# Optimization experiments

Measured on AMD Instinct MI355X. Metric: run time of the kernel, lower is better.

Reference implementation:

```python
import jax, jax.numpy as jnp
import numpy as np

DEPTH = 4  # init kwarg 'depth'
H = 256   # init kwarg 'hidden_size'
ATOM_FDIM, BOND_FDIM = 35, 5


def _build_graph(rng, N, E):
    src = rng.integers(0, N, E).astype(np.int32)
    dst = rng.integers(0, N, E).astype(np.int32)
    # line graph (backtracking=False): lg edge e1 -> e2 iff dst[e1]==src[e2] and src[e1]!=dst[e2]
    indeg = np.bincount(dst, minlength=N)
    idx_sorted = np.argsort(dst, kind='stable')          # edge ids grouped by dst node
    ptr = np.concatenate([[0], np.cumsum(indeg)]).astype(np.int64)
    counts = indeg[src]                                   # in-edges of src[e] feed edge e
    total = int(counts.sum())
    lg_dst = np.repeat(np.arange(E, dtype=np.int64), counts)
    cum = np.cumsum(counts) - counts
    within = np.arange(total) - np.repeat(cum, counts)
    lg_src = idx_sorted[np.repeat(ptr[src], counts) + within]
    keep = src[lg_src] != dst[lg_dst]                     # drop backtracking pairs
    return src, dst, lg_src[keep].astype(np.int32), lg_dst[keep].astype(np.int32)


def setup_inputs() -> dict:
    rng = np.random.default_rng(0)
    N, E, Et, K, G = 50000, 200000, 100000, 50000, 2000
    src, dst, lg_src, lg_dst = _build_graph(rng, N, E)
    graph_ids = ((np.arange(N, dtype=np.int64) * G) // N).astype(np.int32)
    f32 = lambda *s: rng.standard_normal(s).astype(np.float32)
    return {
        'x_nodes': jnp.asarray(f32(N, ATOM_FDIM)),
        'x_edges': jnp.asarray(rng.random((E, BOND_FDIM)).astype(np.float32)),
        'tree_m': jnp.asarray(f32(Et, H) * 0.1),
        'W_i': jnp.asarray(f32(ATOM_FDIM + BOND_FDIM, H) * 0.05),
        'W_h': jnp.asarray(f32(H, H) * 0.05),
        'W_o': jnp.asarray(f32(ATOM_FDIM + H, H) * 0.05),
        'b_o': jnp.asarray(f32(H) * 0.05),
        'edge_src': jnp.asarray(src),
        'edge_dst': jnp.asarray(dst),
        'lg_src': jnp.asarray(lg_src),
        'lg_dst': jnp.asarray(lg_dst),
        'tgt_nodes': jnp.asarray(rng.integers(0, N, K).astype(np.int32)),
        'tree_eid': jnp.asarray(rng.integers(0, Et, K).astype(np.int32)),
        'graph_ids': jnp.asarray(graph_ids),
        'n_graphs': G,
    }


def reference(x_nodes, x_edges, tree_m, W_i, W_h, W_o, b_o,
              edge_src, edge_dst, lg_src, lg_dst, tgt_nodes, tree_eid,
              graph_ids, n_graphs):
    N = x_nodes.shape[0]
    E = x_edges.shape[0]
    # edge input features: [src atom feats | bond feats] @ W_i (no bias)
    msg_input = jnp.concatenate([x_nodes[edge_src], x_edges], axis=1) @ W_i  # [E,H]
    msg = jax.nn.relu(msg_input)
    # tree message alignment: scatter-add tree edge messages onto cand nodes
    node_alpha = jnp.zeros((N, msg.shape[1]), msg.dtype).at[tgt_nodes].add(tree_m[tree_eid])
    edge_alpha = node_alpha[edge_src]  # apply_edges: alpha = src alpha
    # loopy BP over the line graph
    for _ in range(DEPTH - 1):
        accum = jax.ops.segment_sum(msg[lg_src], lg_dst, num_segments=E)  # [E,H]
        msg = jax.nn.relu(msg_input + (accum + edge_alpha) @ W_h)
    # gather: m = sum of incoming edge messages per node
    m = jax.ops.segment_sum(msg, edge_dst, num_segments=N)  # [N,H]
    h = jax.nn.relu(jnp.concatenate([x_nodes, m + node_alpha], axis=1) @ W_o + b_o)
    # mean_nodes per candidate graph
    sums = jax.ops.segment_sum(h, graph_ids, num_segments=n_graphs)
    cnt = jax.ops.segment_sum(jnp.ones((N, 1), h.dtype), graph_ids, num_segments=n_graphs)
    return sums / jnp.maximum(cnt, 1.0)
```

## Files before the change

### kernel.cpp

```cpp
#include <hip/hip_runtime.h>
#include <stdint.h>

typedef unsigned short u16;
typedef __attribute__((ext_vector_type(8))) short bf16x8;
typedef __attribute__((ext_vector_type(4))) float f32x4;

#define HD 256
#define AST 328
#define CORR_CAP 8192

static __device__ __forceinline__ float b2f(u16 x){
  union{float f; unsigned u;} v; v.u = ((unsigned)x)<<16; return v.f;
}
static __device__ __forceinline__ u16 f2b(float f){
  union{float f; unsigned u;} v; v.f = f;
  unsigned r = v.u + 0x7fffu + ((v.u>>16)&1u);
  return (u16)(r>>16);
}
static __device__ __forceinline__ void acc4(float* a, uint2 v){
  a[0] += b2f((u16)v.x); a[1] += b2f((u16)(v.x>>16));
  a[2] += b2f((u16)v.y); a[3] += b2f((u16)(v.y>>16));
}

__global__ void k_zero_int(int* __restrict__ p, int n){
  int i = blockIdx.x*256 + threadIdx.x;
  if (i < n) p[i] = 0;
}

__global__ void k_hist(const int* __restrict__ key, int* __restrict__ deg, int n){
  int i = blockIdx.x*256 + threadIdx.x;
  if (i < n) atomicAdd(&deg[key[i]], 1);
}

__global__ void k_scan_p1(const int* __restrict__ deg, int n, int* __restrict__ bsum){
  int i = blockIdx.x*256 + threadIdx.x;
  int v = (i < n) ? deg[i] : 0;
  #pragma unroll
  for (int o=32; o>0; o>>=1) v += __shfl_down(v, o);
  __shared__ int w[4];
  if ((threadIdx.x&63)==0) w[threadIdx.x>>6] = v;
  __syncthreads();
  if (threadIdx.x==0) bsum[blockIdx.x] = w[0]+w[1]+w[2]+w[3];
}
__global__ __launch_bounds__(1024) void k_scan_p2(int* __restrict__ bsum, int nb,
                                                  int* __restrict__ total_dst){
  __shared__ int sm[1024];
  int t = threadIdx.x;
  int v = (t < nb) ? bsum[t] : 0;
  sm[t] = v; __syncthreads();
  for (int o=1; o<1024; o<<=1){
    int u = (t>=o) ? sm[t-o] : 0;
    __syncthreads();
    sm[t] += u;
    __syncthreads();
  }
  if (t < nb) bsum[t] = sm[t] - v;
  if (t == 1023 && total_dst) *total_dst = sm[1023];
}
__global__ void k_scan_p3(const int* __restrict__ deg, const int* __restrict__ bsum, int n,
                          int* __restrict__ start, int* __restrict__ cursor){
  int t = threadIdx.x;
  int i = blockIdx.x*256 + t;
  int v = (i < n) ? deg[i] : 0;
  __shared__ int sm[256];
  sm[t] = v; __syncthreads();
  for (int o=1; o<256; o<<=1){
    int u = (t>=o) ? sm[t-o] : 0;
    __syncthreads();
    sm[t] += u;
    __syncthreads();
  }
  int ex = sm[t] - v + bsum[blockIdx.x];
  if (i < n){ start[i] = ex; cursor[i] = ex; }
}

__global__ void k_fill(const int* __restrict__ key, const int* __restrict__ val,
                       int* __restrict__ cursor, int* __restrict__ bucket, int n){
  int i = blockIdx.x*256 + threadIdx.x;
  if (i >= n) return;
  int pos = atomicAdd(&cursor[key[i]], 1);
  bucket[pos] = val ? val[i] : i;
}

__global__ void k_permarr(const int* __restrict__ perm, const int* __restrict__ esrc,
                          const int* __restrict__ edst, int* __restrict__ esrc_p,
                          int* __restrict__ edst_p, int E){
  int e = blockIdx.x*256 + threadIdx.x;
  if (e >= E) return;
  int o = perm[e];
  esrc_p[e] = esrc[o];
  edst_p[e] = edst[o];
}

__global__ void k_feat_e(const float* __restrict__ xn, const float* __restrict__ xe,
                         const int* __restrict__ perm, const int* __restrict__ esrc_p,
                         u16* __restrict__ feat, int E){
  int g = blockIdx.x*256 + threadIdx.x;
  int e = g >> 6, c = g & 63;
  if (e >= E) return;
  float v = 0.f;
  if (c < 35) v = xn[(size_t)esrc_p[e]*35 + c];
  else if (c < 40) v = xe[(size_t)perm[e]*5 + (c-35)];
  feat[g] = f2b(v);
}
__global__ void k_xnf(const float* __restrict__ xn, u16* __restrict__ xnf, int N){
  int g = blockIdx.x*256 + threadIdx.x;
  int v2 = g >> 6, c = g & 63;
  if (v2 >= N) return;
  float v = (c < 35) ? xn[(size_t)v2*35 + c] : 0.f;
  xnf[g] = f2b(v);
}

__global__ void k_alpha_gather(const float* __restrict__ tree_m, const int* __restrict__ start,
                               const int* __restrict__ bucket, u16* __restrict__ alpha16, int N){
  int v = (int)(((long long)blockIdx.x*blockDim.x + threadIdx.x)>>6);
  int l = threadIdx.x & 63;
  if (v >= N) return;
  int s = start[v], e2 = start[v+1];
  float a0=0.f,a1=0.f,a2=0.f,a3=0.f;
  for (int j=s;j<e2;j++){
    float4 tv = *(const float4*)(tree_m + (size_t)bucket[j]*HD + l*4);
    a0 += tv.x; a1 += tv.y; a2 += tv.z; a3 += tv.w;
  }
  ushort4 o; o.x=f2b(a0); o.y=f2b(a1); o.z=f2b(a2); o.w=f2b(a3);
  *(ushort4*)(alpha16 + (size_t)v*HD + l*4) = o;
}

__global__ void k_nodesum(const u16* __restrict__ msg, const u16* __restrict__ alpha16,
                          const int* __restrict__ start_d, u16* __restrict__ nodeacc, int N){
  int v = (int)(((long long)blockIdx.x*blockDim.x + threadIdx.x)>>6);
  int l = threadIdx.x & 63;
  if (v >= N) return;
  int s = start_d[v], e2 = start_d[v+1];
  float a[4];
  { uint2 av = *(const uint2*)(alpha16 + (size_t)v*HD + l*4);
    a[0]=b2f((u16)av.x); a[1]=b2f((u16)(av.x>>16));
    a[2]=b2f((u16)av.y); a[3]=b2f((u16)(av.y>>16)); }
  const u16* ml = msg + (size_t)s*HD + l*4;
  int cnt = e2 - s;
  int j = 0;
  for (; j+2 <= cnt; j+=2){
    uint2 v0 = *(const uint2*)(ml);
    uint2 v1 = *(const uint2*)(ml + HD);
    ml += 2*HD;
    acc4(a, v0); acc4(a, v1);
  }
  for (; j < cnt; j++){
    uint2 v0 = *(const uint2*)(ml); ml += HD;
    acc4(a, v0);
  }
  ushort4 o; o.x=f2b(a[0]); o.y=f2b(a[1]); o.z=f2b(a[2]); o.w=f2b(a[3]);
  *(ushort4*)(nodeacc + (size_t)v*HD + l*4) = o;
}

__global__ void k_pairs(const int* __restrict__ esrc_p, const int* __restrict__ edst_p,
                        const int* __restrict__ start_d,
                        int* __restrict__ npairs, int2* __restrict__ pairs, int E){
  int e = blockIdx.x*256 + threadIdx.x;
  if (e >= E) return;
  int u = esrc_p[e], v = edst_p[e];
  int s = start_d[u], t = start_d[u+1];
  for (int ep=s; ep<t; ep++){
    if (esrc_p[ep] == v){
      int pos = atomicAdd(npairs, 1);
      if (pos < CORR_CAP) pairs[pos] = (int2){e, ep};
    }
  }
}

__global__ void k_snapshot(const u16* __restrict__ msg, const int2* __restrict__ pairs,
                           const int* __restrict__ npairs_p, u16* __restrict__ corrbuf){
  int np = *npairs_p; if (np > CORR_CAP) np = CORR_CAP;
  int wid = (blockIdx.x*256 + threadIdx.x) >> 6;
  int l = threadIdx.x & 63;
  int nw = gridDim.x * 4;
  for (int p = wid; p < np; p += nw){
    int ep = pairs[p].y;
    *(uint2*)(corrbuf + (size_t)p*HD + l*4) =
        *(const uint2*)(msg + (size_t)ep*HD + l*4);
  }
}

__global__ __launch_bounds__(256) void k_fixup(
    const float* __restrict__ xn, const float* __restrict__ xe,
    const int* __restrict__ perm, const int* __restrict__ esrc_p,
    const u16* __restrict__ nacc, const u16* __restrict__ corrbuf,
    const int2* __restrict__ pairs, const int* __restrict__ npairs_p,
    const float* __restrict__ Wi, const float* __restrict__ Wh, u16* __restrict__ msg){
  int np = *npairs_p; if (np > CORR_CAP) np = CORR_CAP;
  int t = threadIdx.x;
  __shared__ float cs[256];
  for (int p = blockIdx.x; p < np; p += gridDim.x){
    int e = pairs[p].x;
    bool first = true;
    for (int q=0;q<p;q++) if (pairs[q].x == e){ first = false; break; }
    if (!first) continue;
    int u = esrc_p[e];
    float c = 0.f;
    for (int q=p;q<np;q++) if (pairs[q].x == e) c += b2f(corrbuf[(size_t)q*HD + t]);
    cs[t] = c; __syncthreads();
    float acc = 0.f;
    for (int k=0;k<35;k++) acc += xn[(size_t)u*35 + k] * Wi[k*HD + t];
    int oe = perm[e];
    for (int k=0;k<5;k++)  acc += xe[(size_t)oe*5 + k] * Wi[(35+k)*HD + t];
    for (int k=0;k<HD;k++) acc += (b2f(nacc[(size_t)u*HD + k]) - cs[k]) * Wh[k*HD + t];
    msg[(size_t)e*HD + t] = f2b(acc > 0.f ? acc : 0.f);
    __syncthreads();
  }
}

__global__ void k_prep_B(const float* __restrict__ Wi, const float* __restrict__ Wh,
                         const float* __restrict__ Wo,
                         u16* __restrict__ BTf_bp, u16* __restrict__ BTf_fo){
  int g = blockIdx.x*256 + threadIdx.x;
  if (g >= 81920) return;
  int i = g & 7;
  int l = (g>>3) & 63;
  int t = g >> 9;
  int nj = t & 15, ks = t >> 4;
  int n = nj*16 + (l & 15);
  int k = ks*32 + (l>>4)*8 + i;
  float bp = 0.f, fo = 0.f;
  if (k < 40) bp = Wi[k*HD + n];
  else if (k >= 64) bp = Wh[(k-64)*HD + n];
  if (k < 35) fo = Wo[k*HD + n];
  else if (k >= 64) fo = Wo[(k-29)*HD + n];
  BTf_bp[g] = f2b(bp);
  BTf_fo[g] = f2b(fo);
}

__global__ __launch_bounds__(512, 4) void k_mpnn(
    const u16* __restrict__ featA, const u16* __restrict__ nacc,
    const int* __restrict__ esrc,
    const u16* __restrict__ BTf, const float* __restrict__ bias,
    u16* __restrict__ out16, float* __restrict__ out32, int M, int mode)
{
  __shared__ u16 A_lds[16][AST];
  const int tid = threadIdx.x;
  const int w = tid>>6, l = tid&63;
  const int lr = l&15, lq = l>>4;
  const int nks = (mode==0) ? 2 : 10;
  const int nrb = (M+15)>>4;
  const int gstep = gridDim.x;

  bf16x8 Breg0[10], Breg1[10];
  #pragma unroll
  for (int ks=0; ks<10; ks++){
    if (ks < nks){
      Breg0[ks] = *(const bf16x8*)(BTf + (size_t)((ks*16 + w*2    )*512) + l*8);
      Breg1[ks] = *(const bf16x8*)(BTf + (size_t)((ks*16 + w*2 + 1)*512) + l*8);
    }
  }

  const int c0 = (w*2)*16 + lr, c1 = (w*2+1)*16 + lr;
  float b0 = 0.f, b1 = 0.f;
  if (mode == 2){ b0 = bias[c0]; b1 = bias[c1]; }

  uint2 fA={0,0}, fB={0,0}, nA={0,0}, nB={0,0};
  int rb = blockIdx.x;

  if (rb < nrb){
    int rr0 = rb*16 + w*2;
    int r0 = min(rr0, M-1), r1 = min(rr0+1, M-1);
    if (l < 16){
      fA = *(const uint2*)(featA + (size_t)r0*64 + l*4);
      fB = *(const uint2*)(featA + (size_t)r1*64 + l*4);
    }
    if (mode != 0){
      int s0 = esrc ? esrc[r0] : r0;
      int s1 = esrc ? esrc[r1] : r1;
      nA = *(const uint2*)(nacc + (size_t)s0*HD + l*4);
      nB = *(const uint2*)(nacc + (size_t)s1*HD + l*4);
    }
    if (l < 16){
      *(uint2*)&A_lds[w*2  ][l*4] = fA;
      *(uint2*)&A_lds[w*2+1][l*4] = fB;
    }
    if (mode != 0){
      *(uint2*)&A_lds[w*2  ][64 + l*4] = nA;
      *(uint2*)&A_lds[w*2+1][64 + l*4] = nB;
    }
  }
  __syncthreads();

  for (; rb < nrb; rb += gstep){
    int rbn = rb + gstep;
    if (rbn < nrb){
      int rr0 = rbn*16 + w*2;
      int r0 = min(rr0, M-1), r1 = min(rr0+1, M-1);
      if (l < 16){
        fA = *(const uint2*)(featA + (size_t)r0*64 + l*4);
        fB = *(const uint2*)(featA + (size_t)r1*64 + l*4);
      }
      if (mode != 0){
        int s0 = esrc ? esrc[r0] : r0;
        int s1 = esrc ? esrc[r1] : r1;
        nA = *(const uint2*)(nacc + (size_t)s0*HD + l*4);
        nB = *(const uint2*)(nacc + (size_t)s1*HD + l*4);
      }
    }

    f32x4 acc0 = (f32x4){0.f,0.f,0.f,0.f};
    f32x4 acc1 = (f32x4){0.f,0.f,0.f,0.f};
    const u16* Ar = &A_lds[lr][0];
    #pragma unroll
    for (int ks=0; ks<10; ks++){
      if (ks < nks){
        bf16x8 a = *(const bf16x8*)(Ar + ks*32 + lq*8);
        acc0 = __builtin_amdgcn_mfma_f32_16x16x32_bf16(a, Breg0[ks], acc0, 0,0,0);
        acc1 = __builtin_amdgcn_mfma_f32_16x16x32_bf16(a, Breg1[ks], acc1, 0,0,0);
      }
    }

    int m0 = rb*16;
    if (mode == 2){
      #pragma unroll
      for (int reg=0; reg<4; reg++){
        int gm = m0 + lq*4 + reg;
        if (gm < M){
          float v0 = acc0[reg] + b0, v1 = acc1[reg] + b1;
          out32[(size_t)gm*HD + c0] = v0 > 0.f ? v0 : 0.f;
          out32[(size_t)gm*HD + c1] = v1 > 0.f ? v1 : 0.f;
        }
      }
    } else {
      #pragma unroll
      for (int reg=0; reg<4; reg++){
        int gm = m0 + lq*4 + reg;
        if (gm < M){
          float v0 = acc0[reg], v1 = acc1[reg];
          out16[(size_t)gm*HD + c0] = f2b(v0 > 0.f ? v0 : 0.f);
          out16[(size_t)gm*HD + c1] = f2b(v1 > 0.f ? v1 : 0.f);
        }
      }
    }

    __syncthreads();
    if (rbn < nrb){
      if (l < 16){
        *(uint2*)&A_lds[w*2  ][l*4] = fA;
        *(uint2*)&A_lds[w*2+1][l*4] = fB;
      }
      if (mode != 0){
        *(uint2*)&A_lds[w*2  ][64 + l*4] = nA;
        *(uint2*)&A_lds[w*2+1][64 + l*4] = nB;
      }
    }
    __syncthreads();
  }
}

__global__ void k_graph_mean(const float* __restrict__ h, const int* __restrict__ gid,
                             int N, int G, float* __restrict__ out){
  int g = (int)(((long long)blockIdx.x*blockDim.x + threadIdx.x)>>6);
  int l = threadIdx.x & 63;
  if (g >= G) return;
  int lo=0, hi=N;
  while (lo<hi){ int mid=(lo+hi)>>1; if (gid[mid] < g) lo=mid+1; else hi=mid; }
  int b = lo;
  hi = N;
  while (lo<hi){ int mid=(lo+hi)>>1; if (gid[mid] < g+1) lo=mid+1; else hi=mid; }
  int e2 = lo;
  float a0=0.f,a1=0.f,a2=0.f,a3=0.f;
  for (int v=b; v<e2; v++){
    float4 hv = *(const float4*)(h + (size_t)v*HD + l*4);
    a0 += hv.x; a1 += hv.y; a2 += hv.z; a3 += hv.w;
  }
  int cnt = e2 - b; if (cnt < 1) cnt = 1;
  float inv = 1.0f/(float)cnt;
  float4 o; o.x=a0*inv; o.y=a1*inv; o.z=a2*inv; o.w=a3*inv;
  *(float4*)(out + (size_t)g*HD + l*4) = o;
}

extern "C" void kernel_launch(void* const* d_in, const int* in_sizes, int n_in,
                              void* d_out, int out_size, void* d_ws, size_t ws_size,
                              hipStream_t stream){
  const float* x_nodes = (const float*)d_in[0];
  const float* x_edges = (const float*)d_in[1];
  const float* tree_m  = (const float*)d_in[2];
  const float* W_i     = (const float*)d_in[3];
  const float* W_h     = (const float*)d_in[4];
  const float* W_o     = (const float*)d_in[5];
  const float* b_o     = (const float*)d_in[6];
  const int* edge_src = (const int*)d_in[7];
  const int* edge_dst = (const int*)d_in[8];
  const int* tgt      = (const int*)d_in[11];
  const int* teid     = (const int*)d_in[12];
  const int* gid      = (const int*)d_in[13];

  const int N = in_sizes[0]/35;
  const int E = in_sizes[1]/5;
  const int K = in_sizes[11];
  const int G = out_size/HD;

  char* wsb = (char*)d_ws;
  auto align256 = [](size_t x){ return (x + 255) & ~(size_t)255; };
  size_t oMsg    = 0;
  size_t oAlpha  = oMsg    + align256((size_t)E*HD*2);
  size_t oNacc   = oAlpha  + align256((size_t)N*HD*2);
  size_t oFeatE  = oNacc   + align256((size_t)N*HD*2);
  size_t oXnf    = oFeatE  + align256((size_t)E*64*2);
  size_t oBTbp   = oXnf    + align256((size_t)N*64*2);
  size_t oBTfo   = oBTbp   + align256((size_t)81920*2);
  size_t oDegD   = oBTfo   + align256((size_t)81920*2);
  size_t oStartD = oDegD   + align256((size_t)(N+1)*4);
  size_t oCurD   = oStartD + align256((size_t)(N+1)*4);
  size_t oPerm   = oCurD   + align256((size_t)N*4);
  size_t oEsrcP  = oPerm   + align256((size_t)E*4);
  size_t oEdstP  = oEsrcP  + align256((size_t)E*4);
  size_t oDegT   = oEdstP  + align256((size_t)E*4);
  size_t oStartT = oDegT   + align256((size_t)N*4);
  size_t oCurT   = oStartT + align256((size_t)(N+1)*4);
  size_t oBukT   = oCurT   + align256((size_t)N*4);
  size_t oBsum   = oBukT   + align256((size_t)K*4);
  size_t oPairs  = oBsum   + align256((size_t)1024*4);
  size_t oCorrB  = oPairs  + align256((size_t)CORR_CAP*8);

  u16*   msg     = (u16*)(wsb + oMsg);
  u16*   alpha16 = (u16*)(wsb + oAlpha);
  u16*   nacc    = (u16*)(wsb + oNacc);
  u16*   feat_e  = (u16*)(wsb + oFeatE);
  u16*   xnf     = (u16*)(wsb + oXnf);
  u16*   BTf_bp  = (u16*)(wsb + oBTbp);
  u16*   BTf_fo  = (u16*)(wsb + oBTfo);
  int*   deg_d   = (int*)(wsb + oDegD);
  int*   npairs  = deg_d + N;
  int*   start_d = (int*)(wsb + oStartD);
  int*   cur_d   = (int*)(wsb + oCurD);
  int*   perm    = (int*)(wsb + oPerm);
  int*   esrc_p  = (int*)(wsb + oEsrcP);
  int*   edst_p  = (int*)(wsb + oEdstP);
  int*   deg_t   = (int*)(wsb + oDegT);
  int*   start_t = (int*)(wsb + oStartT);
  int*   cur_t   = (int*)(wsb + oCurT);
  int*   buk_t   = (int*)(wsb + oBukT);
  int*   bsum    = (int*)(wsb + oBsum);
  int2*  pairs   = (int2*)(wsb + oPairs);
  u16*   corrbuf = (u16*)(wsb + oCorrB);
  float* hbuf    = (float*)(wsb + oMsg);

  const int egrid256 = (E+255)/256;
  const int kgrid256 = (K+255)/256;
  const int ngrid256 = (N+255)/256;
  const int nbN      = (N+255)/256;

  k_prep_B<<<320, 256, 0, stream>>>(W_i, W_h, W_o, BTf_bp, BTf_fo);

  k_zero_int<<<(N+1+255)/256, 256, 0, stream>>>(deg_d, N+1);
  k_hist<<<egrid256, 256, 0, stream>>>(edge_dst, deg_d, E);
  k_scan_p1<<<nbN, 256, 0, stream>>>(deg_d, N, bsum);
  k_scan_p2<<<1, 1024, 0, stream>>>(bsum, nbN, start_d + N);
  k_scan_p3<<<nbN, 256, 0, stream>>>(deg_d, bsum, N, start_d, cur_d);
  k_fill<<<egrid256, 256, 0, stream>>>(edge_dst, (const int*)0, cur_d, perm, E);
  k_permarr<<<egrid256, 256, 0, stream>>>(perm, edge_src, edge_dst, esrc_p, edst_p, E);
  k_feat_e<<<((size_t)E*64+255)/256, 256, 0, stream>>>(x_nodes, x_edges, perm, esrc_p, feat_e, E);
  k_xnf<<<((size_t)N*64+255)/256, 256, 0, stream>>>(x_nodes, xnf, N);

  k_zero_int<<<ngrid256, 256, 0, stream>>>(deg_t, N);
  k_hist<<<kgrid256, 256, 0, stream>>>(tgt, deg_t, K);
  k_scan_p1<<<nbN, 256, 0, stream>>>(deg_t, N, bsum);
  k_scan_p2<<<1, 1024, 0, stream>>>(bsum, nbN, start_t + N);
  k_scan_p3<<<nbN, 256, 0, stream>>>(deg_t, bsum, N, start_t, cur_t);
  k_fill<<<kgrid256, 256, 0, stream>>>(tgt, teid, cur_t, buk_t, K);
  k_alpha_gather<<<(N+3)/4, 256, 0, stream>>>(tree_m, start_t, buk_t, alpha16, N);

  k_pairs<<<egrid256, 256, 0, stream>>>(esrc_p, edst_p, start_d, npairs, pairs, E);

  k_mpnn<<<512, 512, 0, stream>>>(feat_e, (const u16*)0, (const int*)0,
                                  BTf_bp, (const float*)0, msg, (float*)0, E, 0);
  for (int it=0; it<3; ++it){
    k_nodesum<<<(N+3)/4, 256, 0, stream>>>(msg, alpha16, start_d, nacc, N);
    k_snapshot<<<32, 256, 0, stream>>>(msg, pairs, npairs, corrbuf);
    k_mpnn<<<512, 512, 0, stream>>>(feat_e, nacc, esrc_p,
                                    BTf_bp, (const float*)0, msg, (float*)0, E, 1);
    k_fixup<<<64, 256, 0, stream>>>(x_nodes, x_edges, perm, esrc_p, nacc, corrbuf,
                                    pairs, npairs, W_i, W_h, msg);
  }
  k_nodesum<<<(N+3)/4, 256, 0, stream>>>(msg, alpha16, start_d, nacc, N);
  k_mpnn<<<512, 512, 0, stream>>>(xnf, nacc, (const int*)0,
                                  BTf_fo, b_o, (u16*)0, hbuf, N, 2);
  k_graph_mean<<<(G+3)/4, 256, 0, stream>>>(hbuf, gid, N, G, (float*)d_out);
}
```

Baseline: 655.6 us.

## Hoist per-node GEMMs out of edge loop via linearity, fuse nodesum with GEMM

The W_h and W_i products depend only on the source node, apart from the bond features and a sparse backtracking correction. The change computes them once per node (N rows) instead of once per edge (E rows). A fused node kernel sums incoming messages into LDS and runs the MFMA GEMM against W_h, adding a precomputed x_nodes@W_i term. A light elementwise edge kernel then gathers U[src], adds the 5-wide bond term and applies relu. The risks are that the correction pair capacity drops to 2048, which could truncate fixups, and that rounding changes because the intermediate U is stored as bf16.

```diff
diff --git a/kernel.cpp b/kernel.cpp
--- a/kernel.cpp
+++ b/kernel.cpp
@@ -6,8 +6,8 @@
 typedef __attribute__((ext_vector_type(4))) float f32x4;
 
 #define HD 256
-#define AST 328
-#define CORR_CAP 8192
+#define AST 264
+#define CORR_CAP 2048
 
 static __device__ __forceinline__ float b2f(u16 x){
   union{float f; unsigned u;} v; v.u = ((unsigned)x)<<16; return v.f;
@@ -92,17 +92,15 @@
   edst_p[e] = edst[o];
 }
 
-__global__ void k_feat_e(const float* __restrict__ xn, const float* __restrict__ xe,
-                         const int* __restrict__ perm, const int* __restrict__ esrc_p,
-                         u16* __restrict__ feat, int E){
-  int g = blockIdx.x*256 + threadIdx.x;
-  int e = g >> 6, c = g & 63;
+__global__ void k_xep(const float* __restrict__ xe, const int* __restrict__ perm,
+                      float* __restrict__ xep, int E){
+  int e = blockIdx.x*256 + threadIdx.x;
   if (e >= E) return;
-  float v = 0.f;
-  if (c < 35) v = xn[(size_t)esrc_p[e]*35 + c];
-  else if (c < 40) v = xe[(size_t)perm[e]*5 + (c-35)];
-  feat[g] = f2b(v);
-}
+  int o = perm[e];
+  #pragma unroll
+  for (int k=0;k<5;k++) xep[(size_t)e*5+k] = xe[(size_t)o*5+k];
+}
+
 __global__ void k_xnf(const float* __restrict__ xn, u16* __restrict__ xnf, int N){
   int g = blockIdx.x*256 + threadIdx.x;
   int v2 = g >> 6, c = g & 63;
@@ -126,31 +124,164 @@
   *(ushort4*)(alpha16 + (size_t)v*HD + l*4) = o;
 }
 
-__global__ void k_nodesum(const u16* __restrict__ msg, const u16* __restrict__ alpha16,
-                          const int* __restrict__ start_d, u16* __restrict__ nodeacc, int N){
-  int v = (int)(((long long)blockIdx.x*blockDim.x + threadIdx.x)>>6);
-  int l = threadIdx.x & 63;
-  if (v >= N) return;
-  int s = start_d[v], e2 = start_d[v+1];
-  float a[4];
-  { uint2 av = *(const uint2*)(alpha16 + (size_t)v*HD + l*4);
-    a[0]=b2f((u16)av.x); a[1]=b2f((u16)(av.x>>16));
-    a[2]=b2f((u16)av.y); a[3]=b2f((u16)(av.y>>16)); }
-  const u16* ml = msg + (size_t)s*HD + l*4;
-  int cnt = e2 - s;
-  int j = 0;
-  for (; j+2 <= cnt; j+=2){
-    uint2 v0 = *(const uint2*)(ml);
-    uint2 v1 = *(const uint2*)(ml + HD);
-    ml += 2*HD;
-    acc4(a, v0); acc4(a, v1);
-  }
-  for (; j < cnt; j++){
-    uint2 v0 = *(const uint2*)(ml); ml += HD;
-    acc4(a, v0);
-  }
-  ushort4 o; o.x=f2b(a[0]); o.y=f2b(a[1]); o.z=f2b(a[2]); o.w=f2b(a[3]);
-  *(ushort4*)(nodeacc + (size_t)v*HD + l*4) = o;
+__global__ void k_prep_frag(const float* __restrict__ W, int k0, int kmax, int nks,
+                            u16* __restrict__ out){
+  int g = blockIdx.x*256 + threadIdx.x;
+  if (g >= nks*16*512) return;
+  int i = g & 7, l = (g>>3)&63, t = g>>9;
+  int nj = t & 15, ks = t >> 4;
+  int n = nj*16 + (l&15);
+  int k = ks*32 + (l>>4)*8 + i;
+  float v = (k < kmax) ? W[(size_t)(k0+k)*HD + n] : 0.f;
+  out[g] = f2b(v);
+}
+
+__global__ __launch_bounds__(512, 4) void k_pr_gemm(
+    const u16* __restrict__ featA, const u16* __restrict__ BTf,
+    u16* __restrict__ out16, int M)
+{
+  const int tid = threadIdx.x;
+  const int w = tid>>6, l = tid&63;
+  const int lr = l&15, lq = l>>4;
+  const int nrb = (M+15)>>4;
+  bf16x8 B0[2], B1[2];
+  #pragma unroll
+  for (int ks=0; ks<2; ks++){
+    B0[ks] = *(const bf16x8*)(BTf + (size_t)((ks*16 + w*2  )*512) + l*8);
+    B1[ks] = *(const bf16x8*)(BTf + (size_t)((ks*16 + w*2+1)*512) + l*8);
+  }
+  const int c0 = w*32 + lr, c1 = w*32 + 16 + lr;
+  for (int rb = blockIdx.x; rb < nrb; rb += gridDim.x){
+    int r = rb*16 + lr; int rc = min(r, M-1);
+    const u16* fr = featA + (size_t)rc*64 + lq*8;
+    bf16x8 a0 = *(const bf16x8*)(fr);
+    bf16x8 a1 = *(const bf16x8*)(fr + 32);
+    f32x4 acc0 = (f32x4){0.f,0.f,0.f,0.f};
+    f32x4 acc1 = (f32x4){0.f,0.f,0.f,0.f};
+    acc0 = __builtin_amdgcn_mfma_f32_16x16x32_bf16(a0, B0[0], acc0, 0,0,0);
+    acc0 = __builtin_amdgcn_mfma_f32_16x16x32_bf16(a1, B0[1], acc0, 0,0,0);
+    acc1 = __builtin_amdgcn_mfma_f32_16x16x32_bf16(a0, B1[0], acc1, 0,0,0);
+    acc1 = __builtin_amdgcn_mfma_f32_16x16x32_bf16(a1, B1[1], acc1, 0,0,0);
+    #pragma unroll
+    for (int reg=0; reg<4; reg++){
+      int gm = rb*16 + lq*4 + reg;
+      if (gm < M){
+        out16[(size_t)gm*HD + c0] = f2b(acc0[reg]);
+        out16[(size_t)gm*HD + c1] = f2b(acc1[reg]);
+      }
+    }
+  }
+}
+
+__global__ __launch_bounds__(512, 4) void k_nodeU(
+    const u16* __restrict__ msg, const u16* __restrict__ alpha16,
+    const int* __restrict__ start_d, const u16* __restrict__ BTf,
+    const u16* __restrict__ Padd, const float* __restrict__ bias,
+    u16* __restrict__ out16, float* __restrict__ out32, int N, int mode)
+{
+  __shared__ u16 A_lds[16][AST];
+  const int tid = threadIdx.x;
+  const int w = tid>>6, l = tid&63;
+  const int lr = l&15, lq = l>>4;
+  const int ngrp = (N+15)>>4;
+
+  bf16x8 B0[8], B1[8];
+  #pragma unroll
+  for (int ks=0; ks<8; ks++){
+    B0[ks] = *(const bf16x8*)(BTf + (size_t)((ks*16 + w*2  )*512) + l*8);
+    B1[ks] = *(const bf16x8*)(BTf + (size_t)((ks*16 + w*2+1)*512) + l*8);
+  }
+  const int c0 = w*32 + lr, c1 = w*32 + 16 + lr;
+  float b0 = 0.f, b1 = 0.f;
+  if (mode == 1){ b0 = bias[c0]; b1 = bias[c1]; }
+
+  for (int grp = blockIdx.x; grp < ngrp; grp += gridDim.x){
+    const int vb = grp*16;
+    #pragma unroll
+    for (int h=0; h<2; h++){
+      int v = vb + w*2 + h;
+      float a[4] = {0.f,0.f,0.f,0.f};
+      if (v < N){
+        uint2 av = *(const uint2*)(alpha16 + (size_t)v*HD + l*4);
+        a[0]=b2f((u16)av.x); a[1]=b2f((u16)(av.x>>16));
+        a[2]=b2f((u16)av.y); a[3]=b2f((u16)(av.y>>16));
+        int s = start_d[v], e2 = start_d[v+1];
+        const u16* ml = msg + (size_t)s*HD + l*4;
+        int cnt = e2 - s, j = 0;
+        for (; j+2 <= cnt; j+=2){
+          uint2 v0 = *(const uint2*)(ml);
+          uint2 v1 = *(const uint2*)(ml + HD);
+          ml += 2*HD;
+          acc4(a, v0); acc4(a, v1);
+        }
+        for (; j < cnt; j++){
+          uint2 v0 = *(const uint2*)(ml); ml += HD;
+          acc4(a, v0);
+        }
+      }
+      ushort4 o; o.x=f2b(a[0]); o.y=f2b(a[1]); o.z=f2b(a[2]); o.w=f2b(a[3]);
+      *(ushort4*)&A_lds[w*2+h][l*4] = o;
+    }
+    __syncthreads();
+    f32x4 acc0 = (f32x4){0.f,0.f,0.f,0.f};
+    f32x4 acc1 = (f32x4){0.f,0.f,0.f,0.f};
+    const u16* Ar = &A_lds[lr][0];
+    #pragma unroll
+    for (int ks=0; ks<8; ks++){
+      bf16x8 af = *(const bf16x8*)(Ar + ks*32 + lq*8);
+      acc0 = __builtin_amdgcn_mfma_f32_16x16x32_bf16(af, B0[ks], acc0, 0,0,0);
+      acc1 = __builtin_amdgcn_mfma_f32_16x16x32_bf16(af, B1[ks], acc1, 0,0,0);
+    }
+    #pragma unroll
+    for (int reg=0; reg<4; reg++){
+      int gm = vb + lq*4 + reg;
+      if (gm < N){
+        float v0 = acc0[reg] + b2f(Padd[(size_t)gm*HD + c0]);
+        float v1 = acc1[reg] + b2f(Padd[(size_t)gm*HD + c1]);
+        if (mode == 1){
+          v0 += b0; v1 += b1;
+          out32[(size_t)gm*HD + c0] = v0 > 0.f ? v0 : 0.f;
+          out32[(size_t)gm*HD + c1] = v1 > 0.f ? v1 : 0.f;
+        } else {
+          out16[(size_t)gm*HD + c0] = f2b(v0);
+          out16[(size_t)gm*HD + c1] = f2b(v1);
+        }
+      }
+    }
+    __syncthreads();
+  }
+}
+
+__global__ __launch_bounds__(256, 8) void k_edge_update(
+    const u16* __restrict__ U, const float* __restrict__ xep,
+    const int* __restrict__ esrc_p, const float* __restrict__ Wi,
+    u16* __restrict__ msg, int E)
+{
+  const int l = threadIdx.x & 63;
+  const int wid = (blockIdx.x*256 + threadIdx.x) >> 6;
+  const int nw = gridDim.x*4;
+  float wq[5][4];
+  #pragma unroll
+  for (int k=0;k<5;k++){
+    float4 t = *(const float4*)(Wi + (size_t)(35+k)*HD + l*4);
+    wq[k][0]=t.x; wq[k][1]=t.y; wq[k][2]=t.z; wq[k][3]=t.w;
+  }
+  for (int e = wid; e < E; e += nw){
+    int s = esrc_p[e];
+    const float* xp = xep + (size_t)e*5;
+    float x0=xp[0], x1=xp[1], x2=xp[2], x3=xp[3], x4=xp[4];
+    uint2 uv = *(const uint2*)(U + (size_t)s*HD + l*4);
+    float v[4] = { b2f((u16)uv.x), b2f((u16)(uv.x>>16)),
+                   b2f((u16)uv.y), b2f((u16)(uv.y>>16)) };
+    #pragma unroll
+    for (int j=0;j<4;j++){
+      float q = x0*wq[0][j] + x1*wq[1][j] + x2*wq[2][j] + x3*wq[3][j] + x4*wq[4][j];
+      float r = v[j] + q;
+      v[j] = r > 0.f ? r : 0.f;
+    }
+    ushort4 o; o.x=f2b(v[0]); o.y=f2b(v[1]); o.z=f2b(v[2]); o.w=f2b(v[3]);
+    *(ushort4*)(msg + (size_t)e*HD + l*4) = o;
+  }
 }
 
 __global__ void k_pairs(const int* __restrict__ esrc_p, const int* __restrict__ edst_p,
@@ -182,11 +313,11 @@
 }
 
 __global__ __launch_bounds__(256) void k_fixup(
-    const float* __restrict__ xn, const float* __restrict__ xe,
-    const int* __restrict__ perm, const int* __restrict__ esrc_p,
-    const u16* __restrict__ nacc, const u16* __restrict__ corrbuf,
-    const int2* __restrict__ pairs, const int* __restrict__ npairs_p,
-    const float* __restrict__ Wi, const float* __restrict__ Wh, u16* __restrict__ msg){
+    const u16* __restrict__ U, const float* __restrict__ xep,
+    const int* __restrict__ esrc_p,
+    const u16* __restrict__ corrbuf, const int2* __restrict__ pairs,
+    const int* __restrict__ npairs_p, const float* __restrict__ Wi,
+    const float* __restrict__ Wh, u16* __restrict__ msg){
   int np = *npairs_p; if (np > CORR_CAP) np = CORR_CAP;
   int t = threadIdx.x;
   __shared__ float cs[256];
@@ -195,157 +326,17 @@
     bool first = true;
     for (int q=0;q<p;q++) if (pairs[q].x == e){ first = false; break; }
     if (!first) continue;
-    int u = esrc_p[e];
     float c = 0.f;
     for (int q=p;q<np;q++) if (pairs[q].x == e) c += b2f(corrbuf[(size_t)q*HD + t]);
     cs[t] = c; __syncthreads();
-    float acc = 0.f;
-    for (int k=0;k<35;k++) acc += xn[(size_t)u*35 + k] * Wi[k*HD + t];
-    int oe = perm[e];
-    for (int k=0;k<5;k++)  acc += xe[(size_t)oe*5 + k] * Wi[(35+k)*HD + t];
-    for (int k=0;k<HD;k++) acc += (b2f(nacc[(size_t)u*HD + k]) - cs[k]) * Wh[k*HD + t];
-    msg[(size_t)e*HD + t] = f2b(acc > 0.f ? acc : 0.f);
-    __syncthreads();
-  }
-}
-
-__global__ void k_prep_B(const float* __restrict__ Wi, const float* __restrict__ Wh,
-                         const float* __restrict__ Wo,
-                         u16* __restrict__ BTf_bp, u16* __restrict__ BTf_fo){
-  int g = blockIdx.x*256 + threadIdx.x;
-  if (g >= 81920) return;
-  int i = g & 7;
-  int l = (g>>3) & 63;
-  int t = g >> 9;
-  int nj = t & 15, ks = t >> 4;
-  int n = nj*16 + (l & 15);
-  int k = ks*32 + (l>>4)*8 + i;
-  float bp = 0.f, fo = 0.f;
-  if (k < 40) bp = Wi[k*HD + n];
-  else if (k >= 64) bp = Wh[(k-64)*HD + n];
-  if (k < 35) fo = Wo[k*HD + n];
-  else if (k >= 64) fo = Wo[(k-29)*HD + n];
-  BTf_bp[g] = f2b(bp);
-  BTf_fo[g] = f2b(fo);
-}
-
-__global__ __launch_bounds__(512, 4) void k_mpnn(
-    const u16* __restrict__ featA, const u16* __restrict__ nacc,
-    const int* __restrict__ esrc,
-    const u16* __restrict__ BTf, const float* __restrict__ bias,
-    u16* __restrict__ out16, float* __restrict__ out32, int M, int mode)
-{
-  __shared__ u16 A_lds[16][AST];
-  const int tid = threadIdx.x;
-  const int w = tid>>6, l = tid&63;
-  const int lr = l&15, lq = l>>4;
-  const int nks = (mode==0) ? 2 : 10;
-  const int nrb = (M+15)>>4;
-  const int gstep = gridDim.x;
-
-  bf16x8 Breg0[10], Breg1[10];
-  #pragma unroll
-  for (int ks=0; ks<10; ks++){
-    if (ks < nks){
-      Breg0[ks] = *(const bf16x8*)(BTf + (size_t)((ks*16 + w*2    )*512) + l*8);
-      Breg1[ks] = *(const bf16x8*)(BTf + (size_t)((ks*16 + w*2 + 1)*512) + l*8);
-    }
-  }
-
-  const int c0 = (w*2)*16 + lr, c1 = (w*2+1)*16 + lr;
-  float b0 = 0.f, b1 = 0.f;
-  if (mode == 2){ b0 = bias[c0]; b1 = bias[c1]; }
-
-  uint2 fA={0,0}, fB={0,0}, nA={0,0}, nB={0,0};
-  int rb = blockIdx.x;
-
-  if (rb < nrb){
-    int rr0 = rb*16 + w*2;
-    int r0 = min(rr0, M-1), r1 = min(rr0+1, M-1);
-    if (l < 16){
-      fA = *(const uint2*)(featA + (size_t)r0*64 + l*4);
-      fB = *(const uint2*)(featA + (size_t)r1*64 + l*4);
-    }
-    if (mode != 0){
-      int s0 = esrc ? esrc[r0] : r0;
-      int s1 = esrc ? esrc[r1] : r1;
-      nA = *(const uint2*)(nacc + (size_t)s0*HD + l*4);
-      nB = *(const uint2*)(nacc + (size_t)s1*HD + l*4);
-    }
-    if (l < 16){
-      *(uint2*)&A_lds[w*2  ][l*4] = fA;
-      *(uint2*)&A_lds[w*2+1][l*4] = fB;
-    }
-    if (mode != 0){
-      *(uint2*)&A_lds[w*2  ][64 + l*4] = nA;
-      *(uint2*)&A_lds[w*2+1][64 + l*4] = nB;
-    }
-  }
-  __syncthreads();
-
-  for (; rb < nrb; rb += gstep){
-    int rbn = rb + gstep;
-    if (rbn < nrb){
-      int rr0 = rbn*16 + w*2;
-      int r0 = min(rr0, M-1), r1 = min(rr0+1, M-1);
-      if (l < 16){
-        fA = *(const uint2*)(featA + (size_t)r0*64 + l*4);
-        fB = *(const uint2*)(featA + (size_t)r1*64 + l*4);
-      }
-      if (mode != 0){
-        int s0 = esrc ? esrc[r0] : r0;
-        int s1 = esrc ? esrc[r1] : r1;
-        nA = *(const uint2*)(nacc + (size_t)s0*HD + l*4);
-        nB = *(const uint2*)(nacc + (size_t)s1*HD + l*4);
-      }
-    }
-
-    f32x4 acc0 = (f32x4){0.f,0.f,0.f,0.f};
-    f32x4 acc1 = (f32x4){0.f,0.f,0.f,0.f};
-    const u16* Ar = &A_lds[lr][0];
-    #pragma unroll
-    for (int ks=0; ks<10; ks++){
-      if (ks < nks){
-        bf16x8 a = *(const bf16x8*)(Ar + ks*32 + lq*8);
-        acc0 = __builtin_amdgcn_mfma_f32_16x16x32_bf16(a, Breg0[ks], acc0, 0,0,0);
-        acc1 = __builtin_amdgcn_mfma_f32_16x16x32_bf16(a, Breg1[ks], acc1, 0,0,0);
-      }
-    }
-
-    int m0 = rb*16;
-    if (mode == 2){
-      #pragma unroll
-      for (int reg=0; reg<4; reg++){
-        int gm = m0 + lq*4 + reg;
-        if (gm < M){
-          float v0 = acc0[reg] + b0, v1 = acc1[reg] + b1;
-          out32[(size_t)gm*HD + c0] = v0 > 0.f ? v0 : 0.f;
-          out32[(size_t)gm*HD + c1] = v1 > 0.f ? v1 : 0.f;
-        }
-      }
-    } else {
-      #pragma unroll
-      for (int reg=0; reg<4; reg++){
-        int gm = m0 + lq*4 + reg;
-        if (gm < M){
-          float v0 = acc0[reg], v1 = acc1[reg];
-          out16[(size_t)gm*HD + c0] = f2b(v0 > 0.f ? v0 : 0.f);
-          out16[(size_t)gm*HD + c1] = f2b(v1 > 0.f ? v1 : 0.f);
-        }
-      }
-    }
-
-    __syncthreads();
-    if (rbn < nrb){
-      if (l < 16){
-        *(uint2*)&A_lds[w*2  ][l*4] = fA;
-        *(uint2*)&A_lds[w*2+1][l*4] = fB;
-      }
-      if (mode != 0){
-        *(uint2*)&A_lds[w*2  ][64 + l*4] = nA;
-        *(uint2*)&A_lds[w*2+1][64 + l*4] = nB;
-      }
-    }
+    float corr = 0.f;
+    for (int k=0;k<HD;k++) corr += cs[k]*Wh[(size_t)k*HD + t];
+    const float* xp = xep + (size_t)e*5;
+    float qv = 0.f;
+    for (int k=0;k<5;k++) qv += xp[k]*Wi[(size_t)(35+k)*HD + t];
+    int u = esrc_p[e];
+    float val = b2f(U[(size_t)u*HD + t]) + qv - corr;
+    msg[(size_t)e*HD + t] = f2b(val > 0.f ? val : 0.f);
     __syncthreads();
   }
 }
@@ -397,12 +388,16 @@
   auto align256 = [](size_t x){ return (x + 255) & ~(size_t)255; };
   size_t oMsg    = 0;
   size_t oAlpha  = oMsg    + align256((size_t)E*HD*2);
-  size_t oNacc   = oAlpha  + align256((size_t)N*HD*2);
-  size_t oFeatE  = oNacc   + align256((size_t)N*HD*2);
-  size_t oXnf    = oFeatE  + align256((size_t)E*64*2);
-  size_t oBTbp   = oXnf    + align256((size_t)N*64*2);
-  size_t oBTfo   = oBTbp   + align256((size_t)81920*2);
-  size_t oDegD   = oBTfo   + align256((size_t)81920*2);
+  size_t oU      = oAlpha  + align256((size_t)N*HD*2);
+  size_t oP      = oU      + align256((size_t)N*HD*2);
+  size_t oR      = oP      + align256((size_t)N*HD*2);
+  size_t oXnf    = oR      + align256((size_t)N*HD*2);
+  size_t oXep    = oXnf    + align256((size_t)N*64*2);
+  size_t oBTP    = oXep    + align256((size_t)E*5*4);
+  size_t oBTWh   = oBTP    + align256((size_t)2*16*512*2);
+  size_t oBTRa   = oBTWh   + align256((size_t)8*16*512*2);
+  size_t oBTWob  = oBTRa   + align256((size_t)2*16*512*2);
+  size_t oDegD   = oBTWob  + align256((size_t)8*16*512*2);
   size_t oStartD = oDegD   + align256((size_t)(N+1)*4);
   size_t oCurD   = oStartD + align256((size_t)(N+1)*4);
   size_t oPerm   = oCurD   + align256((size_t)N*4);
@@ -418,11 +413,15 @@
 
   u16*   msg     = (u16*)(wsb + oMsg);
   u16*   alpha16 = (u16*)(wsb + oAlpha);
-  u16*   nacc    = (u16*)(wsb + oNacc);
-  u16*   feat_e  = (u16*)(wsb + oFeatE);
+  u16*   U       = (u16*)(wsb + oU);
+  u16*   P       = (u16*)(wsb + oP);
+  u16*   R       = (u16*)(wsb + oR);
   u16*   xnf     = (u16*)(wsb + oXnf);
-  u16*   BTf_bp  = (u16*)(wsb + oBTbp);
-  u16*   BTf_fo  = (u16*)(wsb + oBTfo);
+  float* xep     = (float*)(wsb + oXep);
+  u16*   BT_P    = (u16*)(wsb + oBTP);
+  u16*   BT_Wh   = (u16*)(wsb + oBTWh);
+  u16*   BT_Ra   = (u16*)(wsb + oBTRa);
+  u16*   BT_Wob  = (u16*)(wsb + oBTWob);
   int*   deg_d   = (int*)(wsb + oDegD);
   int*   npairs  = deg_d + N;
   int*   start_d = (int*)(wsb + oStartD);
@@ -437,14 +436,17 @@
   int*   bsum    = (int*)(wsb + oBsum);
   int2*  pairs   = (int2*)(wsb + oPairs);
   u16*   corrbuf = (u16*)(wsb + oCorrB);
-  float* hbuf    = (float*)(wsb + oMsg);
+  float* hbuf    = (float*)(wsb + oU);
 
   const int egrid256 = (E+255)/256;
   const int kgrid256 = (K+255)/256;
   const int ngrid256 = (N+255)/256;
   const int nbN      = (N+255)/256;
 
-  k_prep_B<<<320, 256, 0, stream>>>(W_i, W_h, W_o, BTf_bp, BTf_fo);
+  k_prep_frag<<<64,  256, 0, stream>>>(W_i, 0, 35, 2, BT_P);
+  k_prep_frag<<<256, 256, 0, stream>>>(W_h, 0, 256, 8, BT_Wh);
+  k_prep_frag<<<64,  256, 0, stream>>>(W_o, 0, 35, 2, BT_Ra);
+  k_prep_frag<<<256, 256, 0, stream>>>(W_o, 35, 256, 8, BT_Wob);
 
   k_zero_int<<<(N+1+255)/256, 256, 0, stream>>>(deg_d, N+1);
   k_hist<<<egrid256, 256, 0, stream>>>(edge_dst, deg_d, E);
@@ -453,7 +455,7 @@
   k_scan_p3<<<nbN, 256, 0, stream>>>(deg_d, bsum, N, start_d, cur_d);
   k_fill<<<egrid256, 256, 0, stream>>>(edge_dst, (const int*)0, cur_d, perm, E);
   k_permarr<<<egrid256, 256, 0, stream>>>(perm, edge_src, edge_dst, esrc_p, edst_p, E);
-  k_feat_e<<<((size_t)E*64+255)/256, 256, 0, stream>>>(x_nodes, x_edges, perm, esrc_p, feat_e, E);
+  k_xep<<<egrid256, 256, 0, stream>>>(x_edges, perm, xep, E);
   k_xnf<<<((size_t)N*64+255)/256, 256, 0, stream>>>(x_nodes, xnf, N);
 
   k_zero_int<<<ngrid256, 256, 0, stream>>>(deg_t, N);
@@ -466,18 +468,21 @@
 
   k_pairs<<<egrid256, 256, 0, stream>>>(esrc_p, edst_p, start_d, npairs, pairs, E);
 
-  k_mpnn<<<512, 512, 0, stream>>>(feat_e, (const u16*)0, (const int*)0,
-                                  BTf_bp, (const float*)0, msg, (float*)0, E, 0);
+  k_pr_gemm<<<512, 512, 0, stream>>>(xnf, BT_P, P, N);
+  k_pr_gemm<<<512, 512, 0, stream>>>(xnf, BT_Ra, R, N);
+
+  k_edge_update<<<2048, 256, 0, stream>>>(P, xep, esrc_p, W_i, msg, E);
+
   for (int it=0; it<3; ++it){
-    k_nodesum<<<(N+3)/4, 256, 0, stream>>>(msg, alpha16, start_d, nacc, N);
+    k_nodeU<<<512, 512, 0, stream>>>(msg, alpha16, start_d, BT_Wh, P,
+                                     (const float*)0, U, (float*)0, N, 0);
     k_snapshot<<<32, 256, 0, stream>>>(msg, pairs, npairs, corrbuf);
-    k_mpnn<<<512, 512, 0, stream>>>(feat_e, nacc, esrc_p,
-                                    BTf_bp, (const float*)0, msg, (float*)0, E, 1);
-    k_fixup<<<64, 256, 0, stream>>>(x_nodes, x_edges, perm, esrc_p, nacc, corrbuf,
-                                    pairs, npairs, W_i, W_h, msg);
-  }
-  k_nodesum<<<(N+3)/4, 256, 0, stream>>>(msg, alpha16, start_d, nacc, N);
-  k_mpnn<<<512, 512, 0, stream>>>(xnf, nacc, (const int*)0,
-                                  BTf_fo, b_o, (u16*)0, hbuf, N, 2);
+    k_edge_update<<<2048, 256, 0, stream>>>(U, xep, esrc_p, W_i, msg, E);
+    k_fixup<<<64, 256, 0, stream>>>(U, xep, esrc_p, corrbuf, pairs, npairs,
+                                    W_i, W_h, msg);
+  }
+
+  k_nodeU<<<512, 512, 0, stream>>>(msg, alpha16, start_d, BT_Wob, R,
+                                   b_o, (u16*)0, hbuf, N, 1);
   k_graph_mean<<<(G+3)/4, 256, 0, stream>>>(hbuf, gid, N, G, (float*)d_out);
 }
```

Measured after the change: 640.0 us. 1.02x faster.
